# Kernel tuning notes

Hardware: AMD Instinct MI355X
Metric: run time of the kernel (lower is better)

The kernel has to match this reference:

```python
import jax, jax.numpy as jnp
import numpy as np

DIM = 512
N_HEADS = 8
HEAD_DIM = DIM // N_HEADS
KERNEL = 31
HALF_K = KERNEL // 2  # 15
EPS = 1e-5


def setup_inputs() -> dict:
    key = jax.random.key(0)
    ks = jax.random.split(key, 6)
    B, L, D = 2, 2048, DIM
    x = jax.random.normal(ks[0], (B, L, D), dtype=jnp.float32)
    # torch nn.Linear(dim, 3*dim): y = x @ W.T + b; store transposed for x @ W
    Wqkv = jax.random.normal(ks[1], (D, 3 * D), dtype=jnp.float32) * (1.0 / np.sqrt(D))
    bqkv = jnp.zeros((3 * D,), dtype=jnp.float32)
    Wproj = jax.random.normal(ks[2], (D, D), dtype=jnp.float32) * (1.0 / np.sqrt(D))
    bproj = jnp.zeros((D,), dtype=jnp.float32)
    gamma = jnp.ones((D,), dtype=jnp.float32)
    beta = jnp.zeros((D,), dtype=jnp.float32)
    return {"x": x, "Wqkv": Wqkv, "bqkv": bqkv, "Wproj": Wproj,
            "bproj": bproj, "gamma": gamma, "beta": beta}


def reference(x, Wqkv, bqkv, Wproj, bproj, gamma, beta):
    B, L, D = x.shape
    residual = x
    qkv = x @ Wqkv + bqkv                                  # (B, L, 3D)
    qkv = qkv.reshape(B, L, 3, N_HEADS, HEAD_DIM)
    q = jnp.transpose(qkv[:, :, 0], (0, 2, 1, 3))          # (B, H, L, d)
    k = jnp.transpose(qkv[:, :, 1], (0, 2, 1, 3))
    v = jnp.transpose(qkv[:, :, 2], (0, 2, 1, 3))

    # sliding-window band mask: |i - j| <= half_k (dilation == 1)
    pos = jnp.arange(L)
    mask = jnp.abs(pos[None, :] - pos[:, None]) <= HALF_K  # (L, L)

    scale = HEAD_DIM ** -0.5
    attn = jnp.einsum('bhqd,bhkd->bhqk', q, k) * scale     # (B, H, L, L)
    attn = jnp.where(mask[None, None], attn, -jnp.inf)
    attn = jax.nn.softmax(attn, axis=-1)
    attn = jnp.nan_to_num(attn, nan=0.0)
    out = jnp.einsum('bhqk,bhkd->bhqd', attn, v)           # (B, H, L, d)
    out = jnp.transpose(out, (0, 2, 1, 3)).reshape(B, L, D)

    out = out @ Wproj + bproj                              # dropout: eval no-op
    y = out + residual
    mu = jnp.mean(y, axis=-1, keepdims=True)
    var = jnp.var(y, axis=-1, keepdims=True)
    return (y - mu) * jax.lax.rsqrt(var + EPS) * gamma + beta
```

## Files before the change

kernel.cpp:

```cpp
#include <hip/hip_runtime.h>

typedef unsigned short u16;
typedef unsigned int u32;
typedef __attribute__((ext_vector_type(8))) short bf16x8;
typedef __attribute__((ext_vector_type(4))) float f32x4;

#define DEV static __device__ __forceinline__

DEV u16 f2b(float x) {
  u32 u = __float_as_uint(x);
  u = (u + 0x7fffu + ((u >> 16) & 1u)) >> 16;
  return (u16)u;
}
DEV float b2f(u16 h) { return __uint_as_float(((u32)h) << 16); }

DEV f32x4 mfma16(bf16x8 a, bf16x8 b, f32x4 c) {
  return __builtin_amdgcn_mfma_f32_16x16x32_bf16(a, b, c, 0, 0, 0);
}

DEV void gload_lds16(const void* g, void* l) {
  __builtin_amdgcn_global_load_lds(
      (const __attribute__((address_space(1))) void*)g,
      (__attribute__((address_space(3))) void*)l, 16, 0, 0);
}

__global__ __launch_bounds__(256) void prep_kernel(
    const float* __restrict__ x, u16* __restrict__ xb,
    const float* __restrict__ Wqkv, u16* __restrict__ wqkvT,
    const float* __restrict__ Wproj, u16* __restrict__ wprojT) {
  __shared__ float tile[32][33];
  const int bid = blockIdx.x;
  const int tid = threadIdx.x;
  if (bid < 1024) {
    size_t i = (size_t)bid * 256 + tid;
    const f32x4 a = *(const f32x4*)(x + i * 8);
    const f32x4 b = *(const f32x4*)(x + i * 8 + 4);
    alignas(16) u16 t[8];
    t[0] = f2b(a[0]); t[1] = f2b(a[1]); t[2] = f2b(a[2]); t[3] = f2b(a[3]);
    t[4] = f2b(b[0]); t[5] = f2b(b[1]); t[6] = f2b(b[2]); t[7] = f2b(b[3]);
    *(bf16x8*)(xb + i * 8) = *(const bf16x8*)t;
    return;
  }
  const float* W;
  u16* WT;
  int R, C, bx, by;
  if (bid < 1024 + 768) {
    W = Wqkv; WT = wqkvT; R = 512; C = 1536;
    bx = (bid - 1024) % 48; by = (bid - 1024) / 48;
  } else {
    W = Wproj; WT = wprojT; R = 512; C = 512;
    bx = (bid - 1792) % 16; by = (bid - 1792) / 16;
  }
  int tx = tid & 31, ty = tid >> 5;
  int r0 = by * 32, c0 = bx * 32;
  for (int rr = ty; rr < 32; rr += 8)
    tile[rr][tx] = W[(size_t)(r0 + rr) * C + c0 + tx];
  __syncthreads();
  for (int rr = ty; rr < 32; rr += 8)
    WT[(size_t)(c0 + rr) * R + r0 + tx] = f2b(tile[tx][rr]);
}

template <int KDIM>
DEV void gemm_mainloop(const u16* __restrict__ A, const u16* __restrict__ Bt,
                       int m0, int n0, u16* As, u16* Bs, f32x4 acc[4][4]) {
  const int tid = threadIdx.x;
  const int lane = tid & 63;
  const int wave = tid >> 6;
  const int rl = lane & 15;
  const int kf = (lane >> 4) << 3;
  const int wrow = (wave >> 1) << 6;
  const int wcol = (wave & 1) << 6;
  const f32x4 fz = {0.f, 0.f, 0.f, 0.f};
  for (int m = 0; m < 4; ++m)
    for (int n = 0; n < 4; ++n) acc[m][n] = fz;

  const int row_c0 = (wave * 64 + lane) >> 2;
  const int ko_c0 = ((wave * 64 + lane) & 3) << 3;
  const int row_c1 = (256 + wave * 64 + lane) >> 2;
  const int ko_c1 = ((256 + wave * 64 + lane) & 3) << 3;

#define STAGE(k0, buf)                                                          \
  do {                                                                          \
    gload_lds16(A + (size_t)(m0 + row_c0) * KDIM + (k0) + ko_c0,                \
                (char*)As + (buf) * 8192 + wave * 1024);                        \
    gload_lds16(Bt + (size_t)(n0 + row_c0) * KDIM + (k0) + ko_c0,               \
                (char*)Bs + (buf) * 8192 + wave * 1024);                        \
    gload_lds16(A + (size_t)(m0 + row_c1) * KDIM + (k0) + ko_c1,                \
                (char*)As + (buf) * 8192 + 4096 + wave * 1024);                 \
    gload_lds16(Bt + (size_t)(n0 + row_c1) * KDIM + (k0) + ko_c1,               \
                (char*)Bs + (buf) * 8192 + 4096 + wave * 1024);                 \
  } while (0)

  STAGE(0, 0);
  __syncthreads();
  int buf = 0;
  for (int k0 = 0; k0 < KDIM; k0 += 32) {
    if (k0 + 32 < KDIM) STAGE(k0 + 32, buf ^ 1);
    const u16* Ab = As + buf * 4096;
    const u16* Bb = Bs + buf * 4096;
    bf16x8 af[4], bv[4];
    for (int m = 0; m < 4; ++m)
      af[m] = *(const bf16x8*)(Ab + (size_t)(wrow + m * 16 + rl) * 32 + kf);
    for (int n = 0; n < 4; ++n)
      bv[n] = *(const bf16x8*)(Bb + (size_t)(wcol + n * 16 + rl) * 32 + kf);
    for (int m = 0; m < 4; ++m)
      for (int n = 0; n < 4; ++n)
        acc[m][n] = mfma16(af[m], bv[n], acc[m][n]);
    __syncthreads();
    buf ^= 1;
  }
#undef STAGE
}

__global__ __launch_bounds__(256) void gemm_qkv_kernel(
    const u16* __restrict__ xb, const u16* __restrict__ wT, const float* __restrict__ bias,
    u16* __restrict__ qb, u16* __restrict__ kb, u16* __restrict__ vb) {
  __shared__ u16 As[2 * 128 * 32];
  __shared__ u16 Bs[2 * 128 * 32];
  f32x4 acc[4][4];
  int m0 = blockIdx.y * 128, n0 = blockIdx.x * 128;
  gemm_mainloop<512>(xb, wT, m0, n0, As, Bs, acc);
  const int lane = threadIdx.x & 63, wave = threadIdx.x >> 6;
  const int wrow = (wave >> 1) << 6, wcol = (wave & 1) << 6;
  const int g = lane >> 4, cl = lane & 15;
  for (int n = 0; n < 4; ++n) {
    int col = n0 + wcol + n * 16 + cl;
    int sid = col >> 9;
    int h = (col >> 6) & 7, d = col & 63;
    u16* dst = sid == 0 ? qb : (sid == 1 ? kb : vb);
    float bvv = bias[col];
    for (int m = 0; m < 4; ++m)
      for (int i = 0; i < 4; ++i) {
        int row = m0 + wrow + m * 16 + g * 4 + i;
        int bb = row >> 11, ll = row & 2047;
        dst[(((size_t)bb * 8 + h) * 2048 + ll) * 64 + d] = f2b(acc[m][n][i] + bvv);
      }
  }
}

__global__ __launch_bounds__(256) void attn_kernel(const u16* __restrict__ qb,
                                                   const u16* __restrict__ kb,
                                                   const u16* __restrict__ vb,
                                                   u16* __restrict__ ao) {
  __shared__ u16 Qs[64 * 72];
  __shared__ u16 Ks[96 * 72];
  __shared__ u16 Vt[64 * 104];
  __shared__ u16 Ps[64 * 104];
  const int tid = threadIdx.x;
  const int bh = blockIdx.y;
  const int q0 = blockIdx.x * 64;
  const int k0s = q0 - 16;
  const u16* qg = qb + ((size_t)bh * 2048 + q0) * 64;
  for (int c = tid; c < 512; c += 256) {
    int r = c >> 3, off = (c & 7) << 3;
    *(bf16x8*)&Qs[r * 72 + off] = *(const bf16x8*)&qg[r * 64 + off];
  }
  const bf16x8 z8 = {0, 0, 0, 0, 0, 0, 0, 0};
  for (int c = tid; c < 768; c += 256) {
    int r = c >> 3, off = (c & 7) << 3;
    int j = k0s + r;
    bf16x8 kv = z8, vv = z8;
    if (j >= 0 && j < 2048) {
      kv = *(const bf16x8*)&kb[((size_t)bh * 2048 + j) * 64 + off];
      vv = *(const bf16x8*)&vb[((size_t)bh * 2048 + j) * 64 + off];
    }
    *(bf16x8*)&Ks[r * 72 + off] = kv;
    const u16* vp = (const u16*)&vv;
    for (int jj = 0; jj < 8; ++jj) Vt[(size_t)(off + jj) * 104 + r] = vp[jj];
  }
  __syncthreads();

  const int w = tid >> 6, l = tid & 63, g = l >> 4, cl = l & 15;
  const f32x4 fz = {0.f, 0.f, 0.f, 0.f};
  f32x4 s[6];
  for (int n = 0; n < 6; ++n) s[n] = fz;
  for (int kk = 0; kk < 64; kk += 32) {
    bf16x8 a = *(const bf16x8*)&Qs[(size_t)(w * 16 + cl) * 72 + kk + g * 8];
    for (int n = 0; n < 6; ++n) {
      bf16x8 b = *(const bf16x8*)&Ks[(size_t)(n * 16 + cl) * 72 + kk + g * 8];
      s[n] = mfma16(a, b, s[n]);
    }
  }
  float pr[6][4];
  for (int i = 0; i < 4; ++i) {
    int qgl = q0 + w * 16 + g * 4 + i;
    float m = -1e30f;
    for (int n = 0; n < 6; ++n) {
      int jg = k0s + n * 16 + cl;
      bool valid = (jg >= 0) && (jg < 2048) && (jg >= qgl - 15) && (jg <= qgl + 15);
      float sv = valid ? s[n][i] * 0.125f : -1e30f;
      pr[n][i] = sv;
      m = fmaxf(m, sv);
    }
    m = fmaxf(m, __shfl_xor(m, 1));
    m = fmaxf(m, __shfl_xor(m, 2));
    m = fmaxf(m, __shfl_xor(m, 4));
    m = fmaxf(m, __shfl_xor(m, 8));
    float sm = 0.f;
    for (int n = 0; n < 6; ++n) {
      float e = __expf(pr[n][i] - m);
      pr[n][i] = e;
      sm += e;
    }
    sm += __shfl_xor(sm, 1);
    sm += __shfl_xor(sm, 2);
    sm += __shfl_xor(sm, 4);
    sm += __shfl_xor(sm, 8);
    float inv = 1.f / sm;
    for (int n = 0; n < 6; ++n)
      Ps[(size_t)(w * 16 + g * 4 + i) * 104 + n * 16 + cl] = f2b(pr[n][i] * inv);
  }
  __syncthreads();

  f32x4 o[4];
  for (int n = 0; n < 4; ++n) o[n] = fz;
  for (int ks = 0; ks < 96; ks += 32) {
    bf16x8 a = *(const bf16x8*)&Ps[(size_t)(w * 16 + cl) * 104 + ks + g * 8];
    for (int n = 0; n < 4; ++n) {
      bf16x8 b = *(const bf16x8*)&Vt[(size_t)(n * 16 + cl) * 104 + ks + g * 8];
      o[n] = mfma16(a, b, o[n]);
    }
  }
  int b_ = bh >> 3, h = bh & 7;
  for (int n = 0; n < 4; ++n)
    for (int i = 0; i < 4; ++i) {
      int qrow = q0 + w * 16 + g * 4 + i;
      ao[((size_t)b_ * 2048 + qrow) * 512 + h * 64 + n * 16 + cl] = f2b(o[n][i]);
    }
}

__global__ __launch_bounds__(256) void gemm_proj_kernel(
    const u16* __restrict__ ab, const u16* __restrict__ wT, const float* __restrict__ bias,
    const float* __restrict__ x, float* __restrict__ y) {
  __shared__ u16 As[2 * 128 * 32];
  __shared__ u16 Bs[2 * 128 * 32];
  f32x4 acc[4][4];
  int m0 = blockIdx.y * 128, n0 = blockIdx.x * 128;
  gemm_mainloop<512>(ab, wT, m0, n0, As, Bs, acc);
  const int lane = threadIdx.x & 63, wave = threadIdx.x >> 6;
  const int wrow = (wave >> 1) << 6, wcol = (wave & 1) << 6;
  const int g = lane >> 4, cl = lane & 15;
  for (int n = 0; n < 4; ++n) {
    int col = n0 + wcol + n * 16 + cl;
    float bvv = bias[col];
    for (int m = 0; m < 4; ++m)
      for (int i = 0; i < 4; ++i) {
        int row = m0 + wrow + m * 16 + g * 4 + i;
        size_t idx = (size_t)row * 512 + col;
        y[idx] = acc[m][n][i] + bvv + x[idx];
      }
  }
}

__global__ __launch_bounds__(256) void ln_kernel(const float* __restrict__ y,
                                                 const float* __restrict__ gamma,
                                                 const float* __restrict__ beta,
                                                 float* __restrict__ out) {
  int row = blockIdx.x * 4 + (threadIdx.x >> 6);
  int lane = threadIdx.x & 63;
  const float* yr = y + (size_t)row * 512 + lane * 8;
  alignas(16) float v[8];
  *(f32x4*)&v[0] = *(const f32x4*)yr;
  *(f32x4*)&v[4] = *(const f32x4*)(yr + 4);
  float sum = 0.f, sq = 0.f;
  for (int j = 0; j < 8; ++j) { sum += v[j]; sq += v[j] * v[j]; }
  for (int d = 1; d < 64; d <<= 1) {
    sum += __shfl_xor(sum, d);
    sq += __shfl_xor(sq, d);
  }
  float mean = sum * (1.f / 512.f);
  float var = sq * (1.f / 512.f) - mean * mean;
  float rstd = rsqrtf(var + 1e-5f);
  int c0 = lane * 8;
  alignas(16) float r[8];
  for (int j = 0; j < 8; ++j) r[j] = (v[j] - mean) * rstd * gamma[c0 + j] + beta[c0 + j];
  float* op = out + (size_t)row * 512 + c0;
  *(f32x4*)&op[0] = *(const f32x4*)&r[0];
  *(f32x4*)&op[4] = *(const f32x4*)&r[4];
}

extern "C" void kernel_launch(void* const* d_in, const int* in_sizes, int n_in,
                              void* d_out, int out_size, void* d_ws, size_t ws_size,
                              hipStream_t stream) {
  const float* x     = (const float*)d_in[0];
  const float* Wqkv  = (const float*)d_in[1];
  const float* bqkv  = (const float*)d_in[2];
  const float* Wproj = (const float*)d_in[3];
  const float* bproj = (const float*)d_in[4];
  const float* gamma = (const float*)d_in[5];
  const float* beta  = (const float*)d_in[6];
  float* out = (float*)d_out;
  char* ws = (char*)d_ws;

  u16* xb     = (u16*)(ws);
  u16* wqkvT  = (u16*)(ws + 4194304);
  u16* wprojT = (u16*)(ws + 5767168);
  u16* qb     = (u16*)(ws + 6291456);
  u16* kb     = (u16*)(ws + 10485760);
  u16* vb     = (u16*)(ws + 14680064);
  u16* ao     = (u16*)(ws + 18874368);
  float* y    = (float*)(ws + 23068672);

  prep_kernel<<<2048, 256, 0, stream>>>(x, xb, Wqkv, wqkvT, Wproj, wprojT);
  gemm_qkv_kernel<<<dim3(12, 32), 256, 0, stream>>>(xb, wqkvT, bqkv, qb, kb, vb);
  attn_kernel<<<dim3(32, 16), 256, 0, stream>>>(qb, kb, vb, ao);
  gemm_proj_kernel<<<dim3(4, 32), 256, 0, stream>>>(ao, wprojT, bproj, x, y);
  ln_kernel<<<1024, 256, 0, stream>>>(y, gamma, beta, out);
}
```

Baseline: 51.88 us.

## Shrink GEMM tiles, swizzle LDS layout, and pipeline loads with explicit waitcnt

Templates the GEMM main loop on tile size and uses smaller tiles (64x128 for QKV, 64x64 for proj), so each grid launches more blocks and fills more of the CU count. It adds an XOR swizzle on the LDS k-offset to cut bank conflicts on fragment reads. It also replaces __syncthreads with explicit vmcnt/lgkmcnt waits and raw barriers so the next stage's loads overlap compute, and raises wave priority around the MFMA block. The smaller tiles give less data reuse per block, and the hand-written waitcnt logic has to match the number of loads issued.

```diff
diff --git a/kernel.cpp b/kernel.cpp
--- a/kernel.cpp
+++ b/kernel.cpp
@@ -43,12 +43,12 @@
   }
   const float* W;
   u16* WT;
-  int R, C, bx, by;
+  int C, bx, by;
   if (bid < 1024 + 768) {
-    W = Wqkv; WT = wqkvT; R = 512; C = 1536;
+    W = Wqkv; WT = wqkvT; C = 1536;
     bx = (bid - 1024) % 48; by = (bid - 1024) / 48;
   } else {
-    W = Wproj; WT = wprojT; R = 512; C = 512;
+    W = Wproj; WT = wprojT; C = 512;
     bx = (bid - 1792) % 16; by = (bid - 1792) / 16;
   }
   int tx = tid & 31, ty = tid >> 5;
@@ -57,71 +57,92 @@
     tile[rr][tx] = W[(size_t)(r0 + rr) * C + c0 + tx];
   __syncthreads();
   for (int rr = ty; rr < 32; rr += 8)
-    WT[(size_t)(c0 + rr) * R + r0 + tx] = f2b(tile[tx][rr]);
-}
-
-template <int KDIM>
+    WT[(size_t)(c0 + rr) * 512 + r0 + tx] = f2b(tile[tx][rr]);
+}
+
+template <int KDIM, int BM, int BN>
 DEV void gemm_mainloop(const u16* __restrict__ A, const u16* __restrict__ Bt,
-                       int m0, int n0, u16* As, u16* Bs, f32x4 acc[4][4]) {
+                       int m0, int n0, u16* __restrict__ As, u16* __restrict__ Bs,
+                       f32x4 (&acc)[BM / 32][BN / 32]) {
+  constexpr int MI = BM / 32, NI = BN / 32;
+  constexpr int ACH = BM / 64, BCH = BN / 64;
+  constexpr int LOADS = ACH + BCH;
+  constexpr int NSTEP = KDIM / 32;
   const int tid = threadIdx.x;
   const int lane = tid & 63;
   const int wave = tid >> 6;
   const int rl = lane & 15;
-  const int kf = (lane >> 4) << 3;
-  const int wrow = (wave >> 1) << 6;
-  const int wcol = (wave & 1) << 6;
+  const int kf_sw = (((lane >> 4) ^ (rl & 3)) << 3);
+  const int wrow = (wave >> 1) * (BM / 2);
+  const int wcol = (wave & 1) * (BN / 2);
   const f32x4 fz = {0.f, 0.f, 0.f, 0.f};
-  for (int m = 0; m < 4; ++m)
-    for (int n = 0; n < 4; ++n) acc[m][n] = fz;
-
-  const int row_c0 = (wave * 64 + lane) >> 2;
-  const int ko_c0 = ((wave * 64 + lane) & 3) << 3;
-  const int row_c1 = (256 + wave * 64 + lane) >> 2;
-  const int ko_c1 = ((256 + wave * 64 + lane) & 3) << 3;
-
-#define STAGE(k0, buf)                                                          \
-  do {                                                                          \
-    gload_lds16(A + (size_t)(m0 + row_c0) * KDIM + (k0) + ko_c0,                \
-                (char*)As + (buf) * 8192 + wave * 1024);                        \
-    gload_lds16(Bt + (size_t)(n0 + row_c0) * KDIM + (k0) + ko_c0,               \
-                (char*)Bs + (buf) * 8192 + wave * 1024);                        \
-    gload_lds16(A + (size_t)(m0 + row_c1) * KDIM + (k0) + ko_c1,                \
-                (char*)As + (buf) * 8192 + 4096 + wave * 1024);                 \
-    gload_lds16(Bt + (size_t)(n0 + row_c1) * KDIM + (k0) + ko_c1,               \
-                (char*)Bs + (buf) * 8192 + 4096 + wave * 1024);                 \
-  } while (0)
-
-  STAGE(0, 0);
-  __syncthreads();
+#pragma unroll
+  for (int m = 0; m < MI; ++m)
+#pragma unroll
+    for (int n = 0; n < NI; ++n) acc[m][n] = fz;
+
+  auto stage = [&](int k0, int buf) {
+#pragma unroll
+    for (int c = 0; c < ACH; ++c) {
+      int f = c * 256 + tid;
+      int row = f >> 2;
+      int ko = (((f & 3) ^ (row & 3)) << 3);
+      gload_lds16(A + (size_t)(m0 + row) * KDIM + k0 + ko,
+                  (char*)As + buf * (BM * 64) + c * 4096 + wave * 1024);
+    }
+#pragma unroll
+    for (int c = 0; c < BCH; ++c) {
+      int f = c * 256 + tid;
+      int row = f >> 2;
+      int ko = (((f & 3) ^ (row & 3)) << 3);
+      gload_lds16(Bt + (size_t)(n0 + row) * KDIM + k0 + ko,
+                  (char*)Bs + buf * (BN * 64) + c * 4096 + wave * 1024);
+    }
+  };
+
+  stage(0, 0);
   int buf = 0;
-  for (int k0 = 0; k0 < KDIM; k0 += 32) {
-    if (k0 + 32 < KDIM) STAGE(k0 + 32, buf ^ 1);
-    const u16* Ab = As + buf * 4096;
-    const u16* Bb = Bs + buf * 4096;
-    bf16x8 af[4], bv[4];
-    for (int m = 0; m < 4; ++m)
-      af[m] = *(const bf16x8*)(Ab + (size_t)(wrow + m * 16 + rl) * 32 + kf);
-    for (int n = 0; n < 4; ++n)
-      bv[n] = *(const bf16x8*)(Bb + (size_t)(wcol + n * 16 + rl) * 32 + kf);
-    for (int m = 0; m < 4; ++m)
-      for (int n = 0; n < 4; ++n)
+#pragma unroll
+  for (int k = 0; k < NSTEP; ++k) {
+    if (k + 1 < NSTEP) {
+      stage((k + 1) * 32, buf ^ 1);
+      asm volatile("s_waitcnt vmcnt(%0)" ::"i"(LOADS) : "memory");
+    } else {
+      asm volatile("s_waitcnt vmcnt(0)" ::: "memory");
+    }
+    __builtin_amdgcn_s_barrier();
+    const u16* Ab = As + buf * (BM * 32);
+    const u16* Bb = Bs + buf * (BN * 32);
+    bf16x8 af[MI], bv[NI];
+#pragma unroll
+    for (int m = 0; m < MI; ++m)
+      af[m] = *(const bf16x8*)(Ab + (size_t)(wrow + m * 16 + rl) * 32 + kf_sw);
+#pragma unroll
+    for (int n = 0; n < NI; ++n)
+      bv[n] = *(const bf16x8*)(Bb + (size_t)(wcol + n * 16 + rl) * 32 + kf_sw);
+    __builtin_amdgcn_s_setprio(1);
+#pragma unroll
+    for (int m = 0; m < MI; ++m)
+#pragma unroll
+      for (int n = 0; n < NI; ++n)
         acc[m][n] = mfma16(af[m], bv[n], acc[m][n]);
-    __syncthreads();
+    __builtin_amdgcn_s_setprio(0);
+    asm volatile("s_waitcnt lgkmcnt(0)" ::: "memory");
+    __builtin_amdgcn_s_barrier();
     buf ^= 1;
   }
-#undef STAGE
 }
 
 __global__ __launch_bounds__(256) void gemm_qkv_kernel(
     const u16* __restrict__ xb, const u16* __restrict__ wT, const float* __restrict__ bias,
     u16* __restrict__ qb, u16* __restrict__ kb, u16* __restrict__ vb) {
-  __shared__ u16 As[2 * 128 * 32];
+  __shared__ u16 As[2 * 64 * 32];
   __shared__ u16 Bs[2 * 128 * 32];
-  f32x4 acc[4][4];
-  int m0 = blockIdx.y * 128, n0 = blockIdx.x * 128;
-  gemm_mainloop<512>(xb, wT, m0, n0, As, Bs, acc);
+  f32x4 acc[2][4];
+  int m0 = blockIdx.y * 64, n0 = blockIdx.x * 128;
+  gemm_mainloop<512, 64, 128>(xb, wT, m0, n0, As, Bs, acc);
   const int lane = threadIdx.x & 63, wave = threadIdx.x >> 6;
-  const int wrow = (wave >> 1) << 6, wcol = (wave & 1) << 6;
+  const int wrow = (wave >> 1) * 32, wcol = (wave & 1) * 64;
   const int g = lane >> 4, cl = lane & 15;
   for (int n = 0; n < 4; ++n) {
     int col = n0 + wcol + n * 16 + cl;
@@ -129,7 +150,7 @@
     int h = (col >> 6) & 7, d = col & 63;
     u16* dst = sid == 0 ? qb : (sid == 1 ? kb : vb);
     float bvv = bias[col];
-    for (int m = 0; m < 4; ++m)
+    for (int m = 0; m < 2; ++m)
       for (int i = 0; i < 4; ++i) {
         int row = m0 + wrow + m * 16 + g * 4 + i;
         int bb = row >> 11, ll = row & 2047;
@@ -232,18 +253,18 @@
 __global__ __launch_bounds__(256) void gemm_proj_kernel(
     const u16* __restrict__ ab, const u16* __restrict__ wT, const float* __restrict__ bias,
     const float* __restrict__ x, float* __restrict__ y) {
-  __shared__ u16 As[2 * 128 * 32];
-  __shared__ u16 Bs[2 * 128 * 32];
-  f32x4 acc[4][4];
-  int m0 = blockIdx.y * 128, n0 = blockIdx.x * 128;
-  gemm_mainloop<512>(ab, wT, m0, n0, As, Bs, acc);
+  __shared__ u16 As[2 * 64 * 32];
+  __shared__ u16 Bs[2 * 64 * 32];
+  f32x4 acc[2][2];
+  int m0 = blockIdx.y * 64, n0 = blockIdx.x * 64;
+  gemm_mainloop<512, 64, 64>(ab, wT, m0, n0, As, Bs, acc);
   const int lane = threadIdx.x & 63, wave = threadIdx.x >> 6;
-  const int wrow = (wave >> 1) << 6, wcol = (wave & 1) << 6;
+  const int wrow = (wave >> 1) * 32, wcol = (wave & 1) * 32;
   const int g = lane >> 4, cl = lane & 15;
-  for (int n = 0; n < 4; ++n) {
+  for (int n = 0; n < 2; ++n) {
     int col = n0 + wcol + n * 16 + cl;
     float bvv = bias[col];
-    for (int m = 0; m < 4; ++m)
+    for (int m = 0; m < 2; ++m)
       for (int i = 0; i < 4; ++i) {
         int row = m0 + wrow + m * 16 + g * 4 + i;
         size_t idx = (size_t)row * 512 + col;
@@ -302,8 +323,8 @@
   float* y    = (float*)(ws + 23068672);
 
   prep_kernel<<<2048, 256, 0, stream>>>(x, xb, Wqkv, wqkvT, Wproj, wprojT);
-  gemm_qkv_kernel<<<dim3(12, 32), 256, 0, stream>>>(xb, wqkvT, bqkv, qb, kb, vb);
+  gemm_qkv_kernel<<<dim3(12, 64), 256, 0, stream>>>(xb, wqkvT, bqkv, qb, kb, vb);
   attn_kernel<<<dim3(32, 16), 256, 0, stream>>>(qb, kb, vb, ao);
-  gemm_proj_kernel<<<dim3(4, 32), 256, 0, stream>>>(ao, wprojT, bproj, x, y);
+  gemm_proj_kernel<<<dim3(8, 64), 256, 0, stream>>>(ao, wprojT, bproj, x, y);
   ln_kernel<<<1024, 256, 0, stream>>>(y, gamma, beta, out);
 }
```

New measurement: 47.25 us. -8.9%, faster.
